# Kernel tuning notes

Measured on AMD Instinct MI355X. Metric: run time of the kernel, lower is better.

Reference implementation:

```python
import jax, jax.numpy as jnp
import numpy as np
from jax import lax

B, L, D, H, NW, NL = 4, 256, 768, 384, 4, 9
WINDOWS = (3, 5, 7, 9)


def setup_inputs() -> dict:
    key = jax.random.key(0)
    ks = jax.random.split(key, 12)
    s = 0.05
    return {
        "seq_out": jax.random.normal(ks[0], (B, L, D), jnp.float32),
        "valid_ids": jax.random.randint(ks[1], (B, L), 0, 2),
        "w_ih_f": jax.random.normal(ks[2], (NW, 4 * H, D), jnp.float32) * s,
        "w_hh_f": jax.random.normal(ks[3], (NW, 4 * H, H), jnp.float32) * s,
        "b_ih_f": jax.random.normal(ks[4], (NW, 4 * H), jnp.float32) * s,
        "b_hh_f": jax.random.normal(ks[5], (NW, 4 * H), jnp.float32) * s,
        "w_ih_b": jax.random.normal(ks[6], (NW, 4 * H, D), jnp.float32) * s,
        "w_hh_b": jax.random.normal(ks[7], (NW, 4 * H, H), jnp.float32) * s,
        "b_ih_b": jax.random.normal(ks[8], (NW, 4 * H), jnp.float32) * s,
        "b_hh_b": jax.random.normal(ks[9], (NW, 4 * H), jnp.float32) * s,
        "lin_w": jax.random.normal(ks[10], (NL, D), jnp.float32) * s,
        "lin_b": jnp.zeros((NL,), jnp.float32),
    }


def _lstm_last(win, mask, W_ih, W_hh, b, reverse):
    # invalid (out-of-range) steps leave the state untouched, so the final
    # carry equals the hidden state after the last valid step (PyTorch LSTM math).
    Bx, Lx, w, Dx = win.shape
    Hh = W_hh.shape[1]

    def step(carry, xm):
        h, c = carry
        x_t, m = xm  # [B,L,D], [L]
        gates = x_t @ W_ih.T + h @ W_hh.T + b  # [B,L,4H], gate order i,f,g,o
        i, f, g, o = jnp.split(gates, 4, axis=-1)
        i = jax.nn.sigmoid(i)
        f = jax.nn.sigmoid(f)
        g = jnp.tanh(g)
        o = jax.nn.sigmoid(o)
        c_new = f * c + i * g
        h_new = o * jnp.tanh(c_new)
        m3 = m[None, :, None]
        return (jnp.where(m3, h_new, h), jnp.where(m3, c_new, c)), None

    init = (jnp.zeros((Bx, Lx, Hh), win.dtype), jnp.zeros((Bx, Lx, Hh), win.dtype))
    (h, _), _ = lax.scan(step, init, (jnp.moveaxis(win, 2, 0), mask.T), reverse=reverse)
    return h


def _window_features(x, w, Wif, Whf, bf, Wib, Whb, bb):
    # Faithful vectorization of windows_sequence: the sorted index_list for
    # position i is the contiguous slice [max(0,i-w//2) .. min(L-1,i+w//2)].
    Bx, Lx, Dx = x.shape
    half = w // 2
    pos = jnp.arange(Lx)[:, None] + jnp.arange(-half, half + 1)[None, :]  # [L,w]
    mask = (pos >= 0) & (pos < Lx)
    idx = jnp.clip(pos, 0, Lx - 1)
    win = x[:, idx, :]  # [B,L,w,D]
    h_f = _lstm_last(win, mask, Wif, Whf, bf, reverse=False)  # fwd dir: last output
    h_b = _lstm_last(win, mask, Wib, Whb, bb, reverse=True)   # bwd dir over reversed window
    return jnp.concatenate([h_f, h_b], axis=-1)  # [B,L,D]


def _valid_scatter(x, valid_ids):
    # Left-pack tokens with valid_ids==1 (the nested Python scatter loop).
    Bx, Lx, Dx = x.shape
    v = valid_ids.astype(jnp.int32)
    dest = jnp.where(v == 1, jnp.cumsum(v, axis=1) - 1, Lx)  # invalid -> pad slot

    def pack(row_x, row_d):
        return jnp.zeros((Lx + 1, Dx), row_x.dtype).at[row_d].set(row_x)[:Lx]

    return jax.vmap(pack)(x, dest)


def reference(seq_out, valid_ids, w_ih_f, w_hh_f, b_ih_f, b_hh_f,
              w_ih_b, w_hh_b, b_ih_b, b_hh_b, lin_w, lin_b):
    x = _valid_scatter(seq_out, valid_ids)  # [B,L,D]; dropout is identity in eval
    locals_ = [
        _window_features(x, WINDOWS[i],
                         w_ih_f[i], w_hh_f[i], b_ih_f[i] + b_hh_f[i],
                         w_ih_b[i], w_hh_b[i], b_ih_b[i] + b_hh_b[i])
        for i in range(NW)
    ]
    muti = jnp.stack(locals_, axis=2)  # [B,L,NW,D]
    # dot-att: query is the (packed) sequence output itself
    attn = jax.nn.softmax(
        jnp.einsum('bld,blwd->blw', x, muti) / jnp.sqrt(jnp.float32(D)), axis=-1)
    local_feat = jnp.einsum('blw,blwd->bld', attn, muti)
    out = x + local_feat
    return out @ lin_w.T + lin_b  # logits [B,L,NL]
```

## Files before the change

kernel.cpp:

```cpp
#include <hip/hip_runtime.h>
#include <math.h>

#define LL 256
#define DD 768
#define HH 384
#define G4 1536
#define NWIN 4
#define NLIN 9
#define NPOS 1024
#define PROJ_N 12288
#define HSTRIDE 520
#define PSLOTS 33

typedef __attribute__((ext_vector_type(8))) short short8;
typedef __attribute__((ext_vector_type(4))) short short4v;
typedef __attribute__((ext_vector_type(16))) float f32x16;

static __device__ __forceinline__ float bf2f(unsigned short u) {
    union { unsigned int i; float f; } v; v.i = ((unsigned int)u) << 16; return v.f;
}
static __device__ __forceinline__ unsigned short f2bf(float f) {
    unsigned int u = __float_as_uint(f);
    u += 0x7fff + ((u >> 16) & 1);
    return (unsigned short)(u >> 16);
}
static __device__ __forceinline__ float fsig(float x) {
    return __builtin_amdgcn_rcpf(1.f + __expf(-x));
}
static __device__ __forceinline__ float ftanh(float x) {
    return 1.f - 2.f * __builtin_amdgcn_rcpf(1.f + __expf(2.f * x));
}

__global__ __launch_bounds__(256) void prep_kernel(
        const float* __restrict__ seq, const int* __restrict__ valid,
        unsigned short* __restrict__ xfrag,
        const float* __restrict__ wihF, const float* __restrict__ wihB,
        unsigned short* __restrict__ wfih,
        const float* __restrict__ whhF, const float* __restrict__ whhB,
        unsigned short* __restrict__ wfhh,
        const float* __restrict__ lin_b, float* __restrict__ out) {
    const int tid = threadIdx.x;
    if (blockIdx.x < 128) {
        const int b = blockIdx.x >> 5;
        const int chunk = blockIdx.x & 31;
        __shared__ int dest[LL];
        __shared__ int wsum[4];
        __shared__ int nvalid;
        const int v = valid[b * LL + tid];
        const unsigned long long m = __ballot(v != 0);
        const int lane = tid & 63, wvi = tid >> 6;
        const int pre = __popcll(m & (((unsigned long long)1 << lane) - 1));
        if (lane == 63) wsum[wvi] = pre + (v ? 1 : 0);
        __syncthreads();
        int base = 0;
#pragma unroll
        for (int k = 0; k < 4; ++k) if (k < wvi) base += wsum[k];
        dest[tid] = v ? (base + pre) : -1;
        if (tid == 0) nvalid = wsum[0] + wsum[1] + wsum[2] + wsum[3];
        __syncthreads();
        const int nv = nvalid;
        for (int l = chunk * 8; l < chunk * 8 + 8; ++l) {
            const int d = dest[l];
            if (d >= 0) {
                const float* src = seq + (size_t)(b * LL + l) * DD;
                const int pos = b * LL + d;
                const int pt = pos >> 5, pl = pos & 31;
                for (int j = tid; j < DD / 8; j += 256) {
                    const float4 v0 = ((const float4*)src)[2 * j];
                    const float4 v1 = ((const float4*)src)[2 * j + 1];
                    short8 pv;
                    pv[0] = (short)f2bf(v0.x); pv[1] = (short)f2bf(v0.y);
                    pv[2] = (short)f2bf(v0.z); pv[3] = (short)f2bf(v0.w);
                    pv[4] = (short)f2bf(v1.x); pv[5] = (short)f2bf(v1.y);
                    pv[6] = (short)f2bf(v1.z); pv[7] = (short)f2bf(v1.w);
                    *(short8*)(xfrag + ((size_t)(pt * 48 + (j >> 1)) * 512 + (pl + 32 * (j & 1)) * 8)) = pv;
                }
            }
            if (l >= nv) {
                const int pos = b * LL + l;
                const int pt = pos >> 5, pl = pos & 31;
                const short8 zv = {};
                for (int j = tid; j < DD / 8; j += 256)
                    *(short8*)(xfrag + ((size_t)(pt * 48 + (j >> 1)) * 512 + (pl + 32 * (j & 1)) * 8)) = zv;
            }
        }
    } else if (blockIdx.x < 896) {
        __shared__ unsigned short lds[32 * 768];
        const int cb = blockIdx.x - 128;
        const int isIH = cb < 384;
        const int vblk = isIH ? cb : (cb - 384);
        const int K = isIH ? DD : HH;
        const float* srcF = isIH ? wihF : whhF;
        const float* srcB = isIH ? wihB : whhB;
        unsigned short* dst = isIH ? wfih : wfhh;
        const int vrow0 = vblk * 32;
        const int chain = vrow0 / G4;
        const int dir = chain >> 2, wi = chain & 3;
        const float* src = (dir ? srcB : srcF) + (size_t)(wi * G4 + (vrow0 % G4)) * K;
        const int total = 32 * K;
        for (int i = tid * 4; i < total; i += 1024) {
            const float4 v = *(const float4*)(src + i);
            lds[i + 0] = f2bf(v.x); lds[i + 1] = f2bf(v.y);
            lds[i + 2] = f2bf(v.z); lds[i + 3] = f2bf(v.w);
        }
        __syncthreads();
        const int nks = K >> 4;
        for (int slot = tid; slot < nks * 64; slot += 256) {
            const int ks = slot >> 6;
            const int lane = slot & 63;
            const int row = lane & 31;
            const int kb = ks * 16 + (lane >> 5) * 8;
            const short8 v = *(const short8*)&lds[row * K + kb];
            *(short8*)(dst + ((size_t)vblk * nks + ks) * 512 + lane * 8) = v;
        }
    } else {
        for (int i = tid; i < NPOS * NLIN; i += 256)
            out[i] = lin_b[i % NLIN];
    }
}

__global__ __launch_bounds__(256) void proj_mfma(
        const unsigned short* __restrict__ xf,
        const unsigned short* __restrict__ wf,
        const float* __restrict__ bihf, const float* __restrict__ bhhf,
        const float* __restrict__ bihb, const float* __restrict__ bhhb,
        unsigned short* __restrict__ proj) {
    __shared__ __align__(16) unsigned short st[4 * 4096];
    const int wv = threadIdx.x >> 6;
    const int lane = threadIdx.x & 63;
    const int colid = lane & 31, hq = lane >> 5;
    const int chain = blockIdx.x & 7;
    const int r8 = blockIdx.x >> 3;
    const int us = r8 % 12;
    const int mtg = r8 / 12;
    const int dir = chain >> 2, wi = chain & 3;

    const unsigned short* bP = wf + (size_t)((chain * 48 + wv * 12 + us) * 48) * 512 + lane * 8;
    const unsigned short* aP = xf + (size_t)(mtg * 4 * 48) * 512 + lane * 8;

    f32x16 acc[4] = {};
#pragma unroll 4
    for (int ks = 0; ks < 48; ++ks) {
        const short8 bv = *(const short8*)(bP + ks * 512);
        const short8 a0 = *(const short8*)(aP + (0 * 48 + ks) * 512);
        const short8 a1 = *(const short8*)(aP + (1 * 48 + ks) * 512);
        const short8 a2 = *(const short8*)(aP + (2 * 48 + ks) * 512);
        const short8 a3 = *(const short8*)(aP + (3 * 48 + ks) * 512);
        acc[0] = __builtin_amdgcn_mfma_f32_32x32x16_bf16(a0, bv, acc[0], 0, 0, 0);
        acc[1] = __builtin_amdgcn_mfma_f32_32x32x16_bf16(a1, bv, acc[1], 0, 0, 0);
        acc[2] = __builtin_amdgcn_mfma_f32_32x32x16_bf16(a2, bv, acc[2], 0, 0, 0);
        acc[3] = __builtin_amdgcn_mfma_f32_32x32x16_bf16(a3, bv, acc[3], 0, 0, 0);
    }
    const int br = wv * HH + us * 32 + colid;
    const float bv = (dir ? bihb : bihf)[wi * G4 + br] + (dir ? bhhb : bhhf)[wi * G4 + br];
#pragma unroll
    for (int i = 0; i < 4; ++i) {
#pragma unroll
        for (int r = 0; r < 16; ++r) {
            const int row = (r & 3) + 8 * (r >> 2) + 4 * hq;
            st[i * 4096 + (row * 32 + colid) * 4 + wv] = f2bf(acc[i][r] + bv);
        }
    }
    __syncthreads();
#pragma unroll
    for (int j = 0; j < 8; ++j) {
        const int idx = j * 256 + threadIdx.x;
        const int i = idx >> 9, rem = idx & 511;
        const int pl = rem >> 4, q = rem & 15;
        const int pos = (mtg * 4 + i) * 32 + pl;
        *(int4*)(proj + (size_t)pos * PROJ_N + chain * G4 + us * 128 + q * 8) =
            ((const int4*)st)[idx];
    }
}

__global__ __launch_bounds__(768, 1) void lstm_fused(
        const unsigned short* __restrict__ Wf,
        const unsigned short* __restrict__ proj,
        unsigned short* __restrict__ hfin) {
    const int p = blockIdx.x & 3, sub = (blockIdx.x >> 2) & 1;
    const int slot = blockIdx.x >> 3;
    const int chainA[4] = {3, 7, 2, 6};
    const int chainB[4] = {0, 4, 1, 5};
    const int chain = (slot < 16) ? chainA[p] : chainB[p];
    const int pt = sub * 16 + (slot & 15);
    const int dir = chain >> 2, wi = chain & 3;
    const int w = 3 + 2 * wi, half = wi + 1;
    const int tid = threadIdx.x;
    const int lane = tid & 63, wv = tid >> 6;
    const int colid = lane & 31, hq = lane >> 5;
    const int uu = wv * 32 + colid;
    const int m0 = pt * 32, b = m0 >> 8, l0 = m0 & 255;

    __shared__ __align__(16) unsigned short Hbuf[2][24 * HSTRIDE];
    __shared__ __align__(16) unsigned short Pring[PSLOTS][1536];
    float c[16];
#pragma unroll
    for (int r = 0; r < 16; ++r) c[r] = 0.f;

    const unsigned int* projU = (const unsigned int*)(proj
        + (size_t)(b * LL) * PROJ_N + chain * G4);
    const unsigned short* Wb = Wf + (size_t)((chain * 48 + wv) * 24) * 512 + lane * 8;
    const int ksp = uu >> 4, khp = (uu >> 3) & 1, jp = uu & 7;
    const int hslot = ksp * HSTRIDE + khp * 256 + jp;

    const int t0 = dir ? (w - 1) : 0;
    for (int i = 0; i < 32; ++i) {
        int src = l0 + i + t0 - half;
        src = src < 0 ? 0 : (src > LL - 1 ? LL - 1 : src);
        ((unsigned int*)&Pring[src % PSLOTS][0])[tid] =
            projU[(size_t)src * (PROJ_N / 2) + tid];
    }
    __syncthreads();

    for (int s = 0; s < w; ++s) {
        const int t = dir ? (w - 1 - s) : s;
        const int tmh = t - half;
        unsigned short* cur = Hbuf[s & 1];
        const unsigned short* prev = Hbuf[(s & 1) ^ 1];

        int nsrc = -1;
        unsigned int pref = 0;
        if (s + 1 < w) {
            const int tn = dir ? (w - 2 - s) : (s + 1);
            nsrc = dir ? (l0 + tn - half) : (l0 + 31 + tn - half);
            nsrc = nsrc < 0 ? 0 : (nsrc > LL - 1 ? LL - 1 : nsrc);
            pref = projU[(size_t)nsrc * (PROJ_N / 2) + tid];
        }

        f32x16 acc0 = {}, acc1 = {}, acc2 = {}, acc3 = {};
        if (s > 0) {
            const unsigned short* Alds = prev + lane * 8;
#pragma unroll 4
            for (int ks = 0; ks < 24; ++ks) {
                const short8 av  = *(const short8*)(Alds + ks * HSTRIDE);
                const short8 bv0 = *(const short8*)(Wb + (size_t)(0 * 288 + ks) * 512);
                const short8 bv1 = *(const short8*)(Wb + (size_t)(1 * 288 + ks) * 512);
                const short8 bv2 = *(const short8*)(Wb + (size_t)(2 * 288 + ks) * 512);
                const short8 bv3 = *(const short8*)(Wb + (size_t)(3 * 288 + ks) * 512);
                acc0 = __builtin_amdgcn_mfma_f32_32x32x16_bf16(av, bv0, acc0, 0, 0, 0);
                acc1 = __builtin_amdgcn_mfma_f32_32x32x16_bf16(av, bv1, acc1, 0, 0, 0);
                acc2 = __builtin_amdgcn_mfma_f32_32x32x16_bf16(av, bv2, acc2, 0, 0, 0);
                acc3 = __builtin_amdgcn_mfma_f32_32x32x16_bf16(av, bv3, acc3, 0, 0, 0);
            }
        }

#pragma unroll
        for (int r = 0; r < 16; ++r) {
            const int row = (r & 3) + 8 * (r >> 2) + 4 * hq;
            const int src = l0 + row + tmh;
            const int cs = src < 0 ? 0 : (src > LL - 1 ? LL - 1 : src);
            unsigned short hv;
            if (src >= 0 && src < LL) {
                const short4v pj = *(const short4v*)&Pring[cs % PSLOTS][uu * 4];
                const float gi = acc0[r] + bf2f((unsigned short)pj[0]);
                const float gf = acc1[r] + bf2f((unsigned short)pj[1]);
                const float gg = acc2[r] + bf2f((unsigned short)pj[2]);
                const float go = acc3[r] + bf2f((unsigned short)pj[3]);
                c[r] = fsig(gf) * c[r] + fsig(gi) * ftanh(gg);
                hv = f2bf(fsig(go) * ftanh(c[r]));
            } else {
                hv = (s == 0) ? (unsigned short)0 : prev[hslot + row * 8];
            }
            cur[hslot + row * 8] = hv;
        }

        if (nsrc >= 0)
            ((unsigned int*)&Pring[nsrc % PSLOTS][0])[tid] = pref;
        __syncthreads();
    }

    const unsigned short* fin = Hbuf[(w - 1) & 1];
    unsigned short* ho = hfin + (size_t)chain * (NPOS * HH) + (size_t)pt * 12288;
#pragma unroll
    for (int i = tid; i < 1536; i += 768) {
        const int ks = i >> 6, off = i & 63;
        *(int4*)(ho + ks * 512 + off * 8) = *(const int4*)(fin + ks * HSTRIDE + off * 8);
    }
}

__global__ __launch_bounds__(192) void attn_scores_kernel(
        const unsigned short* __restrict__ xfrag,
        const unsigned short* __restrict__ hfin,
        float* __restrict__ scores) {
    const int pt = blockIdx.x >> 3, seg = blockIdx.x & 7;
    const int dir = seg >> 2, q = seg & 3;
    const int tid = threadIdx.x;
    const int lane = tid & 63, wv3 = tid >> 6;
    const int pos = lane & 31;
    __shared__ float scp[3][4][32];

    const unsigned short* xb = xfrag + ((size_t)(pt * 48 + 24 * dir)) * 512 + lane * 8;
    const unsigned short* hb0 = hfin + (size_t)(dir * 4) * (NPOS * HH) + (size_t)pt * 12288 + lane * 8;

    float sc4[4] = {0.f, 0.f, 0.f, 0.f};
#pragma unroll
    for (int k = 0; k < 2; ++k) {
        const int ks = q * 6 + wv3 * 2 + k;
        const short8 xv = *(const short8*)(xb + ks * 512);
        float xf[8];
#pragma unroll
        for (int j = 0; j < 8; ++j) xf[j] = bf2f((unsigned short)xv[j]);
#pragma unroll
        for (int wi = 0; wi < 4; ++wi) {
            const short8 hv = *(const short8*)(hb0 + (size_t)wi * (NPOS * HH) + ks * 512);
#pragma unroll
            for (int j = 0; j < 8; ++j)
                sc4[wi] = fmaf(xf[j], bf2f((unsigned short)hv[j]), sc4[wi]);
        }
    }
#pragma unroll
    for (int wi = 0; wi < 4; ++wi) sc4[wi] += __shfl_down(sc4[wi], 32);
    if (lane < 32) {
#pragma unroll
        for (int wi = 0; wi < 4; ++wi) scp[wv3][wi][pos] = sc4[wi];
    }
    __syncthreads();
    if (tid < 32) {
#pragma unroll
        for (int wi = 0; wi < 4; ++wi) {
            const float v = scp[0][wi][tid] + scp[1][wi][tid] + scp[2][wi][tid];
            scores[(((size_t)pt * 8 + seg) * 4 + wi) * 32 + tid] = v;
        }
    }
}

__global__ __launch_bounds__(192) void attn_out2_kernel(
        const unsigned short* __restrict__ xfrag,
        const unsigned short* __restrict__ hfin,
        const float* __restrict__ scores,
        const float* __restrict__ lin_w,
        float* __restrict__ out) {
    const int pt = blockIdx.x >> 3, seg = blockIdx.x & 7;
    const int dir = seg >> 2, q = seg & 3;
    const int tid = threadIdx.x;
    const int lane = tid & 63, wv3 = tid >> 6;
    const int pos = lane & 31, kh = lane >> 5;
    const float inv_sqrt_d = 0.03608439182435161f;
    __shared__ float redp[3][32][10];

    float s[4];
#pragma unroll
    for (int wi = 0; wi < 4; ++wi) {
        float v = 0.f;
#pragma unroll
        for (int s2 = 0; s2 < 8; ++s2)
            v += scores[(((size_t)pt * 8 + s2) * 4 + wi) * 32 + pos];
        s[wi] = v * inv_sqrt_d;
    }
    float mx = fmaxf(fmaxf(s[0], s[1]), fmaxf(s[2], s[3]));
    float denom = 0.f;
    float aw[4];
#pragma unroll
    for (int wi = 0; wi < 4; ++wi) { aw[wi] = __expf(s[wi] - mx); denom += aw[wi]; }
    const float rd = __builtin_amdgcn_rcpf(denom);
#pragma unroll
    for (int wi = 0; wi < 4; ++wi) aw[wi] *= rd;

    const unsigned short* xb = xfrag + ((size_t)(pt * 48 + 24 * dir)) * 512 + lane * 8;
    const unsigned short* hb0 = hfin + (size_t)(dir * 4) * (NPOS * HH) + (size_t)pt * 12288 + lane * 8;

    float rp[9];
#pragma unroll
    for (int r = 0; r < 9; ++r) rp[r] = 0.f;
#pragma unroll
    for (int k = 0; k < 2; ++k) {
        const int ks = q * 6 + wv3 * 2 + k;
        const short8 xv = *(const short8*)(xb + ks * 512);
        float ov[8];
#pragma unroll
        for (int j = 0; j < 8; ++j) ov[j] = bf2f((unsigned short)xv[j]);
#pragma unroll
        for (int wi = 0; wi < 4; ++wi) {
            const short8 hv = *(const short8*)(hb0 + (size_t)wi * (NPOS * HH) + ks * 512);
#pragma unroll
            for (int j = 0; j < 8; ++j)
                ov[j] = fmaf(aw[wi], bf2f((unsigned short)hv[j]), ov[j]);
        }
        const int dbase = dir * 384 + ks * 16 + kh * 8;
#pragma unroll
        for (int r = 0; r < 9; ++r) {
            const float4 lw0 = *(const float4*)(lin_w + r * DD + dbase);
            const float4 lw1 = *(const float4*)(lin_w + r * DD + dbase + 4);
            rp[r] += ov[0] * lw0.x + ov[1] * lw0.y + ov[2] * lw0.z + ov[3] * lw0.w
                   + ov[4] * lw1.x + ov[5] * lw1.y + ov[6] * lw1.z + ov[7] * lw1.w;
        }
    }
#pragma unroll
    for (int r = 0; r < 9; ++r) rp[r] += __shfl_down(rp[r], 32);
    if (lane < 32) {
#pragma unroll
        for (int r = 0; r < 9; ++r) redp[wv3][pos][r] = rp[r];
    }
    __syncthreads();
    if (tid < 96) {
#pragma unroll
        for (int e = 0; e < 3; ++e) {
            const int flat = tid * 3 + e;
            const int p2 = flat / 9, r = flat % 9;
            const float sum = redp[0][p2][r] + redp[1][p2][r] + redp[2][p2][r];
            atomicAdd(&out[(size_t)(pt * 32 + p2) * NLIN + r], sum);
        }
    }
}

extern "C" void kernel_launch(void* const* d_in, const int* in_sizes, int n_in,
                              void* d_out, int out_size, void* d_ws, size_t ws_size,
                              hipStream_t stream) {
    (void)in_sizes; (void)n_in; (void)out_size; (void)ws_size;
    const float* seq   = (const float*)d_in[0];
    const int*   valid = (const int*)d_in[1];
    const float* wih_f = (const float*)d_in[2];
    const float* whh_f = (const float*)d_in[3];
    const float* bih_f = (const float*)d_in[4];
    const float* bhh_f = (const float*)d_in[5];
    const float* wih_b = (const float*)d_in[6];
    const float* whh_b = (const float*)d_in[7];
    const float* bih_b = (const float*)d_in[8];
    const float* bhh_b = (const float*)d_in[9];
    const float* lin_w = (const float*)d_in[10];
    const float* lin_b = (const float*)d_in[11];
    float* out = (float*)d_out;

    unsigned short* xfrag = (unsigned short*)d_ws;
    unsigned short* proj  = xfrag + (size_t)NPOS * DD;
    unsigned short* wfhh  = proj + (size_t)NPOS * PROJ_N;
    unsigned short* wfih  = wfhh + (size_t)4718592;
    unsigned short* hfin  = wfih + (size_t)9437184;
    float* scores = (float*)(hfin + (size_t)3145728);

    prep_kernel<<<897, 256, 0, stream>>>(seq, valid, xfrag,
                                         wih_f, wih_b, wfih,
                                         whh_f, whh_b, wfhh,
                                         lin_b, out);
    proj_mfma<<<768, 256, 0, stream>>>(xfrag, wfih, bih_f, bhh_f, bih_b, bhh_b, proj);
    lstm_fused<<<256, 768, 0, stream>>>(wfhh, proj, hfin);
    attn_scores_kernel<<<256, 192, 0, stream>>>(xfrag, hfin, scores);
    attn_out2_kernel<<<256, 192, 0, stream>>>(xfrag, hfin, scores, lin_w, out);
}
```

Measured before the change: 267.9 us.

## Quantize LSTM recurrent weights and hidden state to FP8 e4m3 for MFMA

Recurrent weights W_hh are converted to FP8 e4m3 with a scale of 16 in the prep kernel. The hidden state in LDS is stored as scaled FP8 so the recurrent matmul uses fp8 MFMA instead of bf16, and accumulators are rescaled by 1/256. This halves weight bandwidth and LDS traffic in the serial recurrence loop. The final hidden state is now written to global memory in bf16 on the last step instead of in a separate copy loop. The cost is much lower precision for the recurrent state and weights, and a software fp8 conversion per element.

After: 323.6 us. +20.8%, slower.

```diff
diff --git a/kernel.cpp b/kernel.cpp
--- a/kernel.cpp
+++ b/kernel.cpp
@@ -11,6 +11,7 @@
 #define PROJ_N 12288
 #define HSTRIDE 520
 #define PSLOTS 33
+#define DQ 0.00390625f
 
 typedef __attribute__((ext_vector_type(8))) short short8;
 typedef __attribute__((ext_vector_type(4))) short short4v;
@@ -29,6 +30,29 @@
 }
 static __device__ __forceinline__ float ftanh(float x) {
     return 1.f - 2.f * __builtin_amdgcn_rcpf(1.f + __expf(2.f * x));
+}
+static __device__ __forceinline__ unsigned char f2e4m3(float f) {
+    unsigned int u = __float_as_uint(f);
+    const unsigned int sg = (u >> 24) & 0x80;
+    u &= 0x7fffffff;
+    if (u < 0x3C800000u) {
+        const float af = __uint_as_float(u);
+        unsigned int d = (unsigned int)__float2uint_rn(af * 512.0f);
+        return (unsigned char)(sg | (d > 8 ? 8u : d));
+    }
+    unsigned int r = u + 0x7ffff + ((u >> 20) & 1);
+    if (r > 0x43E00000u) r = 0x43E00000u;
+    const int e = (int)(r >> 23) - 127;
+    const unsigned int m = (r >> 20) & 7;
+    return (unsigned char)(sg | ((unsigned int)(e + 7) << 3) | m);
+}
+static __device__ __forceinline__ float e4m32f(unsigned char b) {
+    const int e = (b >> 3) & 15;
+    const unsigned int m = b & 7;
+    float f;
+    if (e == 0) f = (float)m * 0.001953125f;
+    else f = __uint_as_float(((unsigned int)(e + 120) << 23) | (m << 20));
+    return (b & 0x80) ? -f : f;
 }
 
 __global__ __launch_bounds__(256) void prep_kernel(
@@ -37,7 +61,7 @@
         const float* __restrict__ wihF, const float* __restrict__ wihB,
         unsigned short* __restrict__ wfih,
         const float* __restrict__ whhF, const float* __restrict__ whhB,
-        unsigned short* __restrict__ wfhh,
+        unsigned char* __restrict__ wfhh8,
         const float* __restrict__ lin_b, float* __restrict__ out) {
     const int tid = threadIdx.x;
     if (blockIdx.x < 128) {
@@ -92,7 +116,6 @@
         const int K = isIH ? DD : HH;
         const float* srcF = isIH ? wihF : whhF;
         const float* srcB = isIH ? wihB : whhB;
-        unsigned short* dst = isIH ? wfih : wfhh;
         const int vrow0 = vblk * 32;
         const int chain = vrow0 / G4;
         const int dir = chain >> 2, wi = chain & 3;
@@ -110,8 +133,18 @@
             const int lane = slot & 63;
             const int row = lane & 31;
             const int kb = ks * 16 + (lane >> 5) * 8;
-            const short8 v = *(const short8*)&lds[row * K + kb];
-            *(short8*)(dst + ((size_t)vblk * nks + ks) * 512 + lane * 8) = v;
+            if (isIH) {
+                const short8 v = *(const short8*)&lds[row * K + kb];
+                *(short8*)(wfih + ((size_t)vblk * nks + ks) * 512 + lane * 8) = v;
+            } else {
+                unsigned long long pk = 0;
+#pragma unroll
+                for (int j = 0; j < 8; ++j) {
+                    const float f = bf2f(lds[row * K + kb + j]) * 16.f;
+                    pk |= (unsigned long long)f2e4m3(f) << (8 * j);
+                }
+                *(unsigned long long*)(wfhh8 + ((size_t)vblk * nks + ks) * 512 + lane * 8) = pk;
+            }
         }
     } else {
         for (int i = tid; i < NPOS * NLIN; i += 256)
@@ -174,7 +207,7 @@
 }
 
 __global__ __launch_bounds__(768, 1) void lstm_fused(
-        const unsigned short* __restrict__ Wf,
+        const unsigned char* __restrict__ Wf8,
         const unsigned short* __restrict__ proj,
         unsigned short* __restrict__ hfin) {
     const int p = blockIdx.x & 3, sub = (blockIdx.x >> 2) & 1;
@@ -191,7 +224,7 @@
     const int uu = wv * 32 + colid;
     const int m0 = pt * 32, b = m0 >> 8, l0 = m0 & 255;
 
-    __shared__ __align__(16) unsigned short Hbuf[2][24 * HSTRIDE];
+    __shared__ __align__(16) unsigned char Hbuf[2][24 * HSTRIDE];
     __shared__ __align__(16) unsigned short Pring[PSLOTS][1536];
     float c[16];
 #pragma unroll
@@ -199,9 +232,10 @@
 
     const unsigned int* projU = (const unsigned int*)(proj
         + (size_t)(b * LL) * PROJ_N + chain * G4);
-    const unsigned short* Wb = Wf + (size_t)((chain * 48 + wv) * 24) * 512 + lane * 8;
+    const unsigned char* Wb = Wf8 + (size_t)((chain * 48 + wv) * 24) * 512 + lane * 8;
     const int ksp = uu >> 4, khp = (uu >> 3) & 1, jp = uu & 7;
     const int hslot = ksp * HSTRIDE + khp * 256 + jp;
+    unsigned short* ho = hfin + (size_t)chain * (NPOS * HH) + (size_t)pt * 12288;
 
     const int t0 = dir ? (w - 1) : 0;
     for (int i = 0; i < 32; ++i) {
@@ -215,8 +249,8 @@
     for (int s = 0; s < w; ++s) {
         const int t = dir ? (w - 1 - s) : s;
         const int tmh = t - half;
-        unsigned short* cur = Hbuf[s & 1];
-        const unsigned short* prev = Hbuf[(s & 1) ^ 1];
+        unsigned char* cur = Hbuf[s & 1];
+        const unsigned char* prev = Hbuf[(s & 1) ^ 1];
 
         int nsrc = -1;
         unsigned int pref = 0;
@@ -229,18 +263,18 @@
 
         f32x16 acc0 = {}, acc1 = {}, acc2 = {}, acc3 = {};
         if (s > 0) {
-            const unsigned short* Alds = prev + lane * 8;
+            const unsigned char* Alds = prev + lane * 8;
 #pragma unroll 4
             for (int ks = 0; ks < 24; ++ks) {
-                const short8 av  = *(const short8*)(Alds + ks * HSTRIDE);
-                const short8 bv0 = *(const short8*)(Wb + (size_t)(0 * 288 + ks) * 512);
-                const short8 bv1 = *(const short8*)(Wb + (size_t)(1 * 288 + ks) * 512);
-                const short8 bv2 = *(const short8*)(Wb + (size_t)(2 * 288 + ks) * 512);
-                const short8 bv3 = *(const short8*)(Wb + (size_t)(3 * 288 + ks) * 512);
-                acc0 = __builtin_amdgcn_mfma_f32_32x32x16_bf16(av, bv0, acc0, 0, 0, 0);
-                acc1 = __builtin_amdgcn_mfma_f32_32x32x16_bf16(av, bv1, acc1, 0, 0, 0);
-                acc2 = __builtin_amdgcn_mfma_f32_32x32x16_bf16(av, bv2, acc2, 0, 0, 0);
-                acc3 = __builtin_amdgcn_mfma_f32_32x32x16_bf16(av, bv3, acc3, 0, 0, 0);
+                const long av  = *(const long*)(Alds + ks * HSTRIDE);
+                const long bv0 = *(const long*)(Wb + (size_t)(0 * 288 + ks) * 512);
+                const long bv1 = *(const long*)(Wb + (size_t)(1 * 288 + ks) * 512);
+                const long bv2 = *(const long*)(Wb + (size_t)(2 * 288 + ks) * 512);
+                const long bv3 = *(const long*)(Wb + (size_t)(3 * 288 + ks) * 512);
+                acc0 = __builtin_amdgcn_mfma_f32_32x32x16_fp8_fp8(av, bv0, acc0, 0, 0, 0);
+                acc1 = __builtin_amdgcn_mfma_f32_32x32x16_fp8_fp8(av, bv1, acc1, 0, 0, 0);
+                acc2 = __builtin_amdgcn_mfma_f32_32x32x16_fp8_fp8(av, bv2, acc2, 0, 0, 0);
+                acc3 = __builtin_amdgcn_mfma_f32_32x32x16_fp8_fp8(av, bv3, acc3, 0, 0, 0);
             }
         }
 
@@ -249,17 +283,23 @@
             const int row = (r & 3) + 8 * (r >> 2) + 4 * hq;
             const int src = l0 + row + tmh;
             const int cs = src < 0 ? 0 : (src > LL - 1 ? LL - 1 : src);
-            unsigned short hv;
+            unsigned char hv;
             if (src >= 0 && src < LL) {
                 const short4v pj = *(const short4v*)&Pring[cs % PSLOTS][uu * 4];
-                const float gi = acc0[r] + bf2f((unsigned short)pj[0]);
-                const float gf = acc1[r] + bf2f((unsigned short)pj[1]);
-                const float gg = acc2[r] + bf2f((unsigned short)pj[2]);
-                const float go = acc3[r] + bf2f((unsigned short)pj[3]);
+                const float gi = acc0[r] * DQ + bf2f((unsigned short)pj[0]);
+                const float gf = acc1[r] * DQ + bf2f((unsigned short)pj[1]);
+                const float gg = acc2[r] * DQ + bf2f((unsigned short)pj[2]);
+                const float go = acc3[r] * DQ + bf2f((unsigned short)pj[3]);
                 c[r] = fsig(gf) * c[r] + fsig(gi) * ftanh(gg);
-                hv = f2bf(fsig(go) * ftanh(c[r]));
+                const float h = fsig(go) * ftanh(c[r]);
+                hv = f2e4m3(h * 16.f);
+                if (s == w - 1)
+                    ho[ksp * 512 + khp * 256 + jp + row * 8] = f2bf(h);
             } else {
-                hv = (s == 0) ? (unsigned short)0 : prev[hslot + row * 8];
+                hv = (s == 0) ? (unsigned char)0 : prev[hslot + row * 8];
+                if (s == w - 1)
+                    ho[ksp * 512 + khp * 256 + jp + row * 8] =
+                        f2bf(e4m32f(hv) * 0.0625f);
             }
             cur[hslot + row * 8] = hv;
         }
@@ -267,14 +307,6 @@
         if (nsrc >= 0)
             ((unsigned int*)&Pring[nsrc % PSLOTS][0])[tid] = pref;
         __syncthreads();
-    }
-
-    const unsigned short* fin = Hbuf[(w - 1) & 1];
-    unsigned short* ho = hfin + (size_t)chain * (NPOS * HH) + (size_t)pt * 12288;
-#pragma unroll
-    for (int i = tid; i < 1536; i += 768) {
-        const int ks = i >> 6, off = i & 63;
-        *(int4*)(ho + ks * 512 + off * 8) = *(const int4*)(fin + ks * HSTRIDE + off * 8);
     }
 }
 
@@ -430,10 +462,10 @@
 
     prep_kernel<<<897, 256, 0, stream>>>(seq, valid, xfrag,
                                          wih_f, wih_b, wfih,
-                                         whh_f, whh_b, wfhh,
+                                         whh_f, whh_b, (unsigned char*)wfhh,
                                          lin_b, out);
     proj_mfma<<<768, 256, 0, stream>>>(xfrag, wfih, bih_f, bhh_f, bih_b, bhh_b, proj);
-    lstm_fused<<<256, 768, 0, stream>>>(wfhh, proj, hfin);
+    lstm_fused<<<256, 768, 0, stream>>>((const unsigned char*)wfhh, proj, hfin);
     attn_scores_kernel<<<256, 192, 0, stream>>>(xfrag, hfin, scores);
     attn_out2_kernel<<<256, 192, 0, stream>>>(xfrag, hfin, scores, lin_w, out);
 }
```
